# Optimization experiments

Hardware: AMD Instinct MI355X
Metric: run time of the kernel (lower is better)

The kernel has to match this reference:

```python
import jax, jax.numpy as jnp
import numpy as np

EPS = 1.1920929e-07  # torch.finfo(torch.float32).eps
R = 2
K = 2 * R - 1  # 3x3 directional kernels

# kornia normalized sobel kernels (divided by sum of |k| = 8)
_SOBEL_X = np.array([[-1.0, 0.0, 1.0], [-2.0, 0.0, 2.0], [-1.0, 0.0, 1.0]], np.float32) / 8.0
_SOBEL_Y = _SOBEL_X.T.copy()


def _conv2d_same(x, k2d, pad_mode):
    """Depthwise 'same' cross-correlation of x:[B,C,H,W] with a single [kh,kw] kernel."""
    B, C, H, W = x.shape
    kh, kw = k2d.shape
    ph, pw = kh // 2, kw // 2
    xp = jnp.pad(x, ((0, 0), (0, 0), (ph, ph), (pw, pw)), mode=pad_mode)
    xr = xp.reshape(B * C, 1, H + 2 * ph, W + 2 * pw)
    kr = jnp.asarray(k2d, x.dtype)[None, None]  # [1,1,kh,kw]
    y = jax.lax.conv_general_dilated(
        xr, kr, window_strides=(1, 1), padding='VALID',
        dimension_numbers=('NCHW', 'OIHW', 'NCHW'))
    return y.reshape(B, C, H, W)


def _spatial_gradient(x):
    # kornia SpatialGradient(mode='sobel', normalized=True) with replicate padding
    gx = _conv2d_same(x, _SOBEL_X, 'edge')
    gy = _conv2d_same(x, _SOBEL_Y, 'edge')
    return gx, gy


def _edge_theta(true_labels):
    gx, gy = _spatial_gradient(true_labels)
    gxx, _ = _spatial_gradient(gx)       # second_grad_x[:, :, 0]
    gxy, gyy = _spatial_gradient(gy)     # second_grad_y[:, :, 0], [:, :, 1]
    theta = jnp.fmod(
        jnp.arctan(gyy * jnp.sign(-gxy + EPS) / (gxx + EPS)),
        np.float32(np.pi))
    return theta


def _directional_kernels():
    vert = np.zeros((K, K), np.float32); vert[:, R - 1] = 1.0   # ones column
    horiz = np.zeros((K, K), np.float32); horiz[R - 1, :] = 1.0  # ones row
    lead = np.eye(K, dtype=np.float32)
    cnt = np.fliplr(np.eye(K, dtype=np.float32)).copy()
    return horiz, vert, lead, cnt


def setup_inputs() -> dict:
    key = jax.random.key(0)
    k1, k2 = jax.random.split(key)
    true_labels = jax.random.uniform(k1, (8, 2, 1024, 1024), dtype=jnp.float32)
    pred_labels = jax.random.normal(k2, (8, 2, 1024, 1024), dtype=jnp.float32)
    return {"true_labels": true_labels, "pred_labels": pred_labels}


def reference(true_labels, pred_labels):
    theta = _edge_theta(true_labels)
    # quantize edge direction into 5 bins
    thresh_theta = jnp.fmod(jnp.round(theta * (5.0 / np.float32(np.pi))) + 5.0, 5.0)
    exp_preds = jnp.exp(pred_labels)

    horiz_k, vert_k, lead_k, cnt_k = _directional_kernels()
    # kornia filter2D default: reflect padding, no normalization
    horiz_f = _conv2d_same(exp_preds, horiz_k, 'reflect')
    vert_f = _conv2d_same(exp_preds, vert_k, 'reflect')
    lead_f = _conv2d_same(exp_preds, lead_k, 'reflect')
    cnt_f = _conv2d_same(exp_preds, cnt_k, 'reflect')

    horiz_nms = (thresh_theta == 0).astype(exp_preds.dtype) * (exp_preds / (horiz_f + EPS))
    vert_nms = (thresh_theta == 2).astype(exp_preds.dtype) * (exp_preds / (vert_f + EPS))
    lead_nms = (thresh_theta == 3).astype(exp_preds.dtype) * (exp_preds / (lead_f + EPS))
    cnt_nms = (thresh_theta == 1).astype(exp_preds.dtype) * (exp_preds / (cnt_f + EPS))

    # cat along new dim then total sum == sum of the four partial sums
    nms_loss = horiz_nms.sum() + vert_nms.sum() + lead_nms.sum() + cnt_nms.sum()
    return nms_loss
```

## Files before the change

### kernel.cpp

```cpp
#include <hip/hip_runtime.h>

#define HHI 1024
#define WWI 1024
#define NI  16
#define HWSZ (HHI * WWI)
#define EPSF  1.1920929e-07f
#define EPS64 7.62939453125e-06f
#define T1 0.3249196962329063f
#define T2 1.3763819204711735f

#define SW 256
#define RW 16
#define GX  (WWI / SW)
#define GYB (HHI / (RW * 4))
#define NB  (GX * GYB * NI)
#define FR_IMG 8176
#define FR_TOT (FR_IMG * NI)

__device__ __forceinline__ int clampi(int v, int hi) { return v < 0 ? 0 : (v > hi ? hi : v); }
__device__ __forceinline__ int refli(int v, int n)  { return v < 0 ? -v : (v >= n ? 2*n-2-v : v); }
__device__ __forceinline__ float frcp(float x) { return __builtin_amdgcn_rcpf(x); }

#define STAGE(POS, IDX, DOPRED, DOOUT) do {                                           \
    const int i_ = (IDX);                                                             \
    {                                                                                 \
        const int gy_ = clampi(Y0 - 2 + i_, HHI - 1);                                 \
        const float* trow_ = timg + (size_t)gy_ * WWI;                                \
        const float4 cq_ = *(const float4*)(trow_ + x0);                              \
        const float2 lo_ = *(const float2*)(trow_ + cm2);                             \
        const float2 hi_ = *(const float2*)(trow_ + cp4);                             \
        float wv_[8];                                                                 \
        wv_[0] = xokl ? lo_.x : cq_.x;                                                \
        wv_[1] = xokl ? lo_.y : cq_.x;                                                \
        wv_[2] = cq_.x; wv_[3] = cq_.y; wv_[4] = cq_.z; wv_[5] = cq_.w;               \
        wv_[6] = xokr ? hi_.x : cq_.w;                                                \
        wv_[7] = xokr ? hi_.y : cq_.w;                                                \
        _Pragma("unroll")                                                             \
        for (int k = 0; k < 4; ++k) {                                                 \
            float s04 = wv_[k] + wv_[k+4];                                            \
            float s13 = wv_[k+1] + wv_[k+3];                                          \
            H1[POS][k] = s04 - 2.f * wv_[k+2];                                        \
            H2[POS][k] = s04 + 4.f * s13 + 6.f * wv_[k+2];                            \
            H3[POS][k] = (wv_[k+4] - wv_[k]) + 2.f * (wv_[k+3] - wv_[k+1]);           \
        }                                                                             \
    }                                                                                 \
    if (DOPRED) {                                                                     \
        const int gp_ = refli(Y0 + i_ - 3, HHI);                                      \
        const float* prow_ = pimg + (size_t)gp_ * WWI;                                \
        const float4 pq_ = *(const float4*)(prow_ + x0);                              \
        const float pl_ = prow_[cm1];                                                 \
        const float pr_ = prow_[cp4s];                                                \
        Ec[POS][0] = __expf(pq_.x); Ec[POS][1] = __expf(pq_.y);                       \
        Ec[POS][2] = __expf(pq_.z); Ec[POS][3] = __expf(pq_.w);                       \
        El[POS] = __expf(xokl ? pl_ : pq_.y);           \
        Er[POS] = __expf(xokr ? pr_ : pq_.z);             \
    }                                                                                 \
    if (DOOUT) {                                                                      \
        const int y_ = Y0 + i_ - 4;                                                   \
        const bool my_ = (y_ >= 2) & (y_ <= HHI - 3);                                 \
        const int q0=(POS+1)%5, q1=(POS+2)%5, q2=(POS+3)%5, q3=(POS+4)%5, q4=POS;     \
        const int e0=(POS+3)%5, e1=(POS+4)%5, e2=POS;                                 \
        _Pragma("unroll")                                                             \
        for (int k = 0; k < 4; ++k) {                                                 \
            float gxx = (H1[q0][k]+H1[q4][k]) + 4.f*(H1[q1][k]+H1[q3][k]) + 6.f*H1[q2][k]; \
            float gyy = (H2[q0][k]+H2[q4][k]) - 2.f*H2[q2][k];                        \
            float gxy = (H3[q4][k]-H3[q0][k]) + 2.f*(H3[q3][k]-H3[q1][k]);            \
            float sarg = EPS64 - gxy;                                                 \
            float num = (sarg > 0.f) ? gyy : ((sarg < 0.f) ? -gyy : 0.f);             \
            float v = num * frcp(gxx + EPS64);                                        \
            bool c2v = (v > T2);                                                      \
            bool c1v = (v > T1) & !c2v;                                               \
            bool c0v = (v >= -T1) & (v <= T1);                                        \
            bool c3v = (v < -T2);                                                     \
            bool have = c2v | c1v | c0v | c3v;                       \
            float r0m = (k==0) ? El[e0] : Ec[e0][(k>0)?k-1:0];                        \
            float r0c = Ec[e0][k];                                                    \
            float r0p = (k==3) ? Er[e0] : Ec[e0][(k<3)?k+1:3];                        \
            float r1m = (k==0) ? El[e1] : Ec[e1][(k>0)?k-1:0];                        \
            float r1c = Ec[e1][k];                                                    \
            float r1p = (k==3) ? Er[e1] : Ec[e1][(k<3)?k+1:3];                        \
            float r2m = (k==0) ? El[e2] : Ec[e2][(k>0)?k-1:0];                        \
            float r2c = Ec[e2][k];                                                    \
            float r2p = (k==3) ? Er[e2] : Ec[e2][(k<3)?k+1:3];                        \
            float d1 = c0v ? r1m : (c2v ? r0c : (c1v ? r0p : r0m));                   \
            float d2 = c0v ? r1p : (c2v ? r2c : (c1v ? r2m : r2p));                   \
            float ec = r1c;                                                           \
            float val = ec * frcp(d1 + ec + d2 + EPSF);                               \
            const int x_ = x0 + k;                                                    \
            bool ok = have & my_ & (x_ >= 2) & (x_ <= WWI - 3);                       \
            term += ok ? val : 0.f;                                                   \
        }                                                                             \
    }                                                                                 \
} while (0)

template <bool USE_WS>
__global__ __launch_bounds__(256, 4) void nms_main(
    const float* __restrict__ tru, const float* __restrict__ prd,
    float* __restrict__ partial)
{
    __shared__ float sred[4];
    const int tid  = threadIdx.x;
    const int lane = tid & 63;
    const int wave = tid >> 6;
    const int z = blockIdx.z;
    const float* timg = tru + (size_t)z * HWSZ;
    const float* pimg = prd + (size_t)z * HWSZ;
    float term = 0.f;

    const int X0 = blockIdx.x * SW;
    const int x0 = X0 + lane * 4;
    const int Y0 = blockIdx.y * (RW * 4) + wave * RW;
    const bool xokl = (x0 >= 2);
    const bool xokr = (x0 + 4 <= WWI - 1);
    const int cm2  = xokl ? x0 - 2 : 0;
    const int cp4  = xokr ? x0 + 4 : WWI - 2;
    const int cm1  = xokl ? x0 - 1 : 0;
    const int cp4s = xokr ? x0 + 4 : WWI - 1;

    float H1[5][4], H2[5][4], H3[5][4];
    float Ec[5][4], El[5], Er[5];

    STAGE(0, 0, 0, 0);
    STAGE(1, 1, 0, 0);
    STAGE(2, 2, 1, 0);
    STAGE(3, 3, 1, 0);
    STAGE(4, 4, 1, 1);
    #pragma unroll 1
    for (int g = 1; g < 4; ++g) {
        const int ib = g * 5;
        STAGE(0, ib + 0, 1, 1);
        STAGE(1, ib + 1, 1, 1);
        STAGE(2, ib + 2, 1, 1);
        STAGE(3, ib + 3, 1, 1);
        STAGE(4, ib + 4, 1, 1);
    }

    {
        const int wid = (((z * gridDim.y) + blockIdx.y) * gridDim.x + blockIdx.x) * 4 + wave;
        int fp = wid * 32 + lane;
        const bool valid = (lane < 32) && (fp < FR_TOT);
        if (fp >= FR_TOT) fp = FR_TOT - 1;
        const int fz = fp / FR_IMG;
        const int p  = fp - fz * FR_IMG;
        const float* ftim = tru + (size_t)fz * HWSZ;
        const float* fpim = prd + (size_t)fz * HWSZ;
        int y, x;
        if (p < 2048)      { y = p >> 10;                   x = p & 1023; }
        else if (p < 4096) { y = 1022 + ((p - 2048) >> 10); x = p & 1023; }
        else { int q = p - 4096; y = 2 + (q >> 2); int xi = q & 3; x = (xi < 2) ? xi : 1020 + xi; }

        int R1[3], C1[3], R2[3][3], C2[3][3];
        #pragma unroll
        for (int a = 0; a < 3; ++a) { R1[a] = clampi(y + a - 1, HHI - 1); C1[a] = clampi(x + a - 1, WWI - 1); }
        #pragma unroll
        for (int a = 0; a < 3; ++a)
            #pragma unroll
            for (int e = 0; e < 3; ++e) {
                R2[a][e] = clampi(R1[a] + e - 1, HHI - 1);
                C2[a][e] = clampi(C1[a] + e - 1, WWI - 1);
            }
        const int hx[3] = {-1, 0, 1}, vx[3] = {1, 2, 1};
        const int hy[3] = {1, 2, 1},  vy[3] = {-1, 0, 1};
        float gxu[3][3], gyu[3][3];
        #pragma unroll
        for (int a = 0; a < 3; ++a)
            #pragma unroll
            for (int b = 0; b < 3; ++b) {
                float sx = 0.f, sy = 0.f;
                #pragma unroll
                for (int e = 0; e < 3; ++e)
                    #pragma unroll
                    for (int f = 0; f < 3; ++f) {
                        const int wx = hx[f] * vx[e], wy = hy[f] * vy[e];
                        if (wx | wy) {
                            float tv = ftim[(size_t)R2[a][e] * WWI + C2[b][f]];
                            if (wx) sx += (float)wx * tv;
                            if (wy) sy += (float)wy * tv;
                        }
                    }
                gxu[a][b] = sx; gyu[a][b] = sy;
            }
        float gxx = 0.f, gxy = 0.f, gyy = 0.f;
        #pragma unroll
        for (int a = 0; a < 3; ++a)
            #pragma unroll
            for (int b = 0; b < 3; ++b) {
                const int w1 = hx[b] * vx[a], w2 = hy[b] * vy[a];
                if (w1) { gxx += (float)w1 * gxu[a][b]; gxy += (float)w1 * gyu[a][b]; }
                if (w2) { gyy += (float)w2 * gyu[a][b]; }
            }
        float sarg = EPS64 - gxy;
        float num = (sarg > 0.f) ? gyy : ((sarg < 0.f) ? -gyy : 0.f);
        float v = num * frcp(gxx + EPS64);
        bool c2v = (v > T2);
        bool c1v = (v > T1) & !c2v;
        bool c0v = (v >= -T1) & (v <= T1);
        bool c3v = (v < -T2);
        bool have = c2v | c1v | c0v | c3v;
        int r1 = c0v ? y : refli(y - 1, HHI);
        int r2 = c0v ? y : refli(y + 1, HHI);
        int xm = refli(x - 1, WWI), xp = refli(x + 1, WWI);
        int co1 = c2v ? x : (c1v ? xp : xm);
        int co2 = c2v ? x : (c1v ? xm : xp);
        float ecf = __expf(fpim[(size_t)y * WWI + x]);
        float d1f = __expf(fpim[(size_t)r1 * WWI + co1]);
        float d2f = __expf(fpim[(size_t)r2 * WWI + co2]);
        float fval = ecf * frcp(d1f + ecf + d2f + EPSF);
        term += (have & valid) ? fval : 0.f;
    }

    for (int off = 32; off; off >>= 1) term += __shfl_down(term, off, 64);
    if (lane == 0) sred[wave] = term;
    __syncthreads();
    if (tid == 0) {
        float b = sred[0] + sred[1] + sred[2] + sred[3];
        if (USE_WS) {
            partial[((size_t)z * gridDim.y + blockIdx.y) * gridDim.x + blockIdx.x] = b;
        } else {
            atomicAdd(partial, b);
        }
    }
}

__global__ __launch_bounds__(1024) void reduce_kernel(
    const float* __restrict__ partial, float* __restrict__ out)
{
    __shared__ float s_red[16];
    float s = 0.f;
    for (int i = threadIdx.x; i < NB; i += 1024) s += partial[i];
    for (int off = 32; off; off >>= 1) s += __shfl_down(s, off, 64);
    if ((threadIdx.x & 63) == 0) s_red[threadIdx.x >> 6] = s;
    __syncthreads();
    if (threadIdx.x == 0) {
        float b = 0.f;
        #pragma unroll
        for (int i = 0; i < 16; ++i) b += s_red[i];
        out[0] = b;
    }
}

extern "C" void kernel_launch(void* const* d_in, const int* in_sizes, int n_in,
                              void* d_out, int out_size, void* d_ws, size_t ws_size,
                              hipStream_t stream) {
    const float* tru = (const float*)d_in[0];
    const float* prd = (const float*)d_in[1];
    float* out = (float*)d_out;
    dim3 grid(GX, GYB, NI);
    dim3 block(256, 1, 1);
    if (ws_size >= (size_t)NB * sizeof(float)) {
        float* ws = (float*)d_ws;
        hipLaunchKernelGGL(nms_main<true>, grid, block, 0, stream, tru, prd, ws);
        hipLaunchKernelGGL(reduce_kernel, dim3(1), dim3(1024), 0, stream, ws, out);
    } else {
        hipMemsetAsync(out, 0, sizeof(float), stream);
        hipLaunchKernelGGL(nms_main<false>, grid, block, 0, stream, tru, prd, out);
    }
}
```

Before: 84.89 us.

## Narrow per-thread strip from four to two columns, doubling thread count

Each lane now handles 2 columns instead of 4, with the block strip width halved to 128, so the grid has twice as many blocks. The register arrays shrink (H arrays to [5][2], and a unified E[5][4] halo replaces the separate Ec/El/Er arrays), which lowers register pressure and raises parallelism. The border fix-up work is respread as 16 lanes per wave because there are more waves. In exchange, the overlapping halo columns are loaded again and exp is recomputed for them relative to the useful work, and loads become float2 instead of float4.

```diff
diff --git a/kernel.cpp b/kernel.cpp
--- a/kernel.cpp
+++ b/kernel.cpp
@@ -9,7 +9,7 @@
 #define T1 0.3249196962329063f
 #define T2 1.3763819204711735f
 
-#define SW 256
+#define SW 128
 #define RW 16
 #define GX  (WWI / SW)
 #define GYB (HHI / (RW * 4))
@@ -26,42 +26,41 @@
     {                                                                                 \
         const int gy_ = clampi(Y0 - 2 + i_, HHI - 1);                                 \
         const float* trow_ = timg + (size_t)gy_ * WWI;                                \
-        const float4 cq_ = *(const float4*)(trow_ + x0);                              \
+        const float2 cq_ = *(const float2*)(trow_ + x0);                              \
         const float2 lo_ = *(const float2*)(trow_ + cm2);                             \
-        const float2 hi_ = *(const float2*)(trow_ + cp4);                             \
-        float wv_[8];                                                                 \
-        wv_[0] = xokl ? lo_.x : cq_.x;                                                \
-        wv_[1] = xokl ? lo_.y : cq_.x;                                                \
-        wv_[2] = cq_.x; wv_[3] = cq_.y; wv_[4] = cq_.z; wv_[5] = cq_.w;               \
-        wv_[6] = xokr ? hi_.x : cq_.w;                                                \
-        wv_[7] = xokr ? hi_.y : cq_.w;                                                \
-        _Pragma("unroll")                                                             \
-        for (int k = 0; k < 4; ++k) {                                                 \
-            float s04 = wv_[k] + wv_[k+4];                                            \
-            float s13 = wv_[k+1] + wv_[k+3];                                          \
-            H1[POS][k] = s04 - 2.f * wv_[k+2];                                        \
-            H2[POS][k] = s04 + 4.f * s13 + 6.f * wv_[k+2];                            \
-            H3[POS][k] = (wv_[k+4] - wv_[k]) + 2.f * (wv_[k+3] - wv_[k+1]);           \
-        }                                                                             \
+        const float2 hi_ = *(const float2*)(trow_ + cp2);                             \
+        const float w0 = xokl ? lo_.x : cq_.x;                                        \
+        const float w1 = xokl ? lo_.y : cq_.x;                                        \
+        const float w2 = cq_.x, w3 = cq_.y;                                           \
+        const float w4 = xokr ? hi_.x : cq_.y;                                        \
+        const float w5 = xokr ? hi_.y : cq_.y;                                        \
+        const float s04 = w0 + w4, s13 = w1 + w3;                                     \
+        H1[POS][0] = s04 - 2.f * w2;                               \
+        H2[POS][0] = s04 + 4.f * s13 + 6.f * w2;                   \
+        H3[POS][0] = (w4 - w0) + 2.f * (w3 - w1);                  \
+        const float t04 = w1 + w5, t13 = w2 + w4;                                     \
+        H1[POS][1] = t04 - 2.f * w3;                                                  \
+        H2[POS][1] = t04 + 4.f * t13 + 6.f * w3;                                      \
+        H3[POS][1] = (w5 - w1) + 2.f * (w4 - w2);                                     \
     }                                                                                 \
     if (DOPRED) {                                                                     \
         const int gp_ = refli(Y0 + i_ - 3, HHI);                                      \
         const float* prow_ = pimg + (size_t)gp_ * WWI;                                \
-        const float4 pq_ = *(const float4*)(prow_ + x0);                              \
-        const float pl_ = prow_[cm1];                                                 \
-        const float pr_ = prow_[cp4s];                                                \
-        Ec[POS][0] = __expf(pq_.x); Ec[POS][1] = __expf(pq_.y);                       \
-        Ec[POS][2] = __expf(pq_.z); Ec[POS][3] = __expf(pq_.w);                       \
-        El[POS] = __expf(xokl ? pl_ : pq_.y);           \
-        Er[POS] = __expf(xokr ? pr_ : pq_.z);             \
+        const float2 pc_ = *(const float2*)(prow_ + x0);                              \
+        const float2 pl_ = *(const float2*)(prow_ + cm2);                             \
+        const float2 ph_ = *(const float2*)(prow_ + cp2);                             \
+        E[POS][0] = __expf(xokl ? pl_.y : pc_.y);          \
+        E[POS][1] = __expf(pc_.x);                                                    \
+        E[POS][2] = __expf(pc_.y);                                                    \
+        E[POS][3] = __expf(xokr ? ph_.x : pc_.x);     \
     }                                                                                 \
     if (DOOUT) {                                                                      \
         const int y_ = Y0 + i_ - 4;                                                   \
         const bool my_ = (y_ >= 2) & (y_ <= HHI - 3);                                 \
         const int q0=(POS+1)%5, q1=(POS+2)%5, q2=(POS+3)%5, q3=(POS+4)%5, q4=POS;     \
-        const int e0=(POS+3)%5, e1=(POS+4)%5, e2=POS;                                 \
+        const int eT=(POS+3)%5, eM=(POS+4)%5, eB=POS;                                 \
         _Pragma("unroll")                                                             \
-        for (int k = 0; k < 4; ++k) {                                                 \
+        for (int k = 0; k < 2; ++k) {                                                 \
             float gxx = (H1[q0][k]+H1[q4][k]) + 4.f*(H1[q1][k]+H1[q3][k]) + 6.f*H1[q2][k]; \
             float gyy = (H2[q0][k]+H2[q4][k]) - 2.f*H2[q2][k];                        \
             float gxy = (H3[q4][k]-H3[q0][k]) + 2.f*(H3[q3][k]-H3[q1][k]);            \
@@ -73,18 +72,9 @@
             bool c0v = (v >= -T1) & (v <= T1);                                        \
             bool c3v = (v < -T2);                                                     \
             bool have = c2v | c1v | c0v | c3v;                       \
-            float r0m = (k==0) ? El[e0] : Ec[e0][(k>0)?k-1:0];                        \
-            float r0c = Ec[e0][k];                                                    \
-            float r0p = (k==3) ? Er[e0] : Ec[e0][(k<3)?k+1:3];                        \
-            float r1m = (k==0) ? El[e1] : Ec[e1][(k>0)?k-1:0];                        \
-            float r1c = Ec[e1][k];                                                    \
-            float r1p = (k==3) ? Er[e1] : Ec[e1][(k<3)?k+1:3];                        \
-            float r2m = (k==0) ? El[e2] : Ec[e2][(k>0)?k-1:0];                        \
-            float r2c = Ec[e2][k];                                                    \
-            float r2p = (k==3) ? Er[e2] : Ec[e2][(k<3)?k+1:3];                        \
-            float d1 = c0v ? r1m : (c2v ? r0c : (c1v ? r0p : r0m));                   \
-            float d2 = c0v ? r1p : (c2v ? r2c : (c1v ? r2m : r2p));                   \
-            float ec = r1c;                                                           \
+            float d1 = c0v ? E[eM][k]   : (c2v ? E[eT][k+1] : (c1v ? E[eT][k+2] : E[eT][k])); \
+            float d2 = c0v ? E[eM][k+2] : (c2v ? E[eB][k+1] : (c1v ? E[eB][k]   : E[eB][k+2])); \
+            float ec = E[eM][k+1];                                                    \
             float val = ec * frcp(d1 + ec + d2 + EPSF);                               \
             const int x_ = x0 + k;                                                    \
             bool ok = have & my_ & (x_ >= 2) & (x_ <= WWI - 3);                       \
@@ -107,18 +97,15 @@
     const float* pimg = prd + (size_t)z * HWSZ;
     float term = 0.f;
 
-    const int X0 = blockIdx.x * SW;
-    const int x0 = X0 + lane * 4;
+    const int x0 = blockIdx.x * SW + lane * 2;
     const int Y0 = blockIdx.y * (RW * 4) + wave * RW;
     const bool xokl = (x0 >= 2);
-    const bool xokr = (x0 + 4 <= WWI - 1);
-    const int cm2  = xokl ? x0 - 2 : 0;
-    const int cp4  = xokr ? x0 + 4 : WWI - 2;
-    const int cm1  = xokl ? x0 - 1 : 0;
-    const int cp4s = xokr ? x0 + 4 : WWI - 1;
-
-    float H1[5][4], H2[5][4], H3[5][4];
-    float Ec[5][4], El[5], Er[5];
+    const bool xokr = (x0 <= WWI - 4);
+    const int cm2 = xokl ? x0 - 2 : 0;
+    const int cp2 = xokr ? x0 + 2 : WWI - 2;
+
+    float H1[5][2], H2[5][2], H3[5][2];
+    float E[5][4];
 
     STAGE(0, 0, 0, 0);
     STAGE(1, 1, 0, 0);
@@ -137,8 +124,8 @@
 
     {
         const int wid = (((z * gridDim.y) + blockIdx.y) * gridDim.x + blockIdx.x) * 4 + wave;
-        int fp = wid * 32 + lane;
-        const bool valid = (lane < 32) && (fp < FR_TOT);
+        int fp = wid * 16 + lane;
+        const bool valid = (lane < 16) && (fp < FR_TOT);
         if (fp >= FR_TOT) fp = FR_TOT - 1;
         const int fz = fp / FR_IMG;
         const int p  = fp - fz * FR_IMG;
```

New measurement: 79.78 us. 1.06x faster.
